# Kernel tuning notes

Hardware: AMD Instinct MI355X
Metric: run time of the kernel (lower is better)

Reference implementation:

```python
import jax, jax.numpy as jnp
import numpy as np

SEQ, D_IN, D_OUT = 8192, 1024, 1024

def setup_inputs() -> dict:
    key = jax.random.key(0)
    kx, kq, kk, kv = jax.random.split(key, 4)
    scale = 1.0 / np.sqrt(D_IN)
    return {
        "x": jax.random.normal(kx, (SEQ, D_IN), dtype=jnp.float32),
        "Wq": jax.random.normal(kq, (D_OUT, D_IN), dtype=jnp.float32) * scale,
        "Wk": jax.random.normal(kk, (D_OUT, D_IN), dtype=jnp.float32) * scale,
        "Wv": jax.random.normal(kv, (D_OUT, D_IN), dtype=jnp.float32) * scale,
    }

def reference(x, Wq, Wk, Wv):
    # nn.Linear: y = x @ W.T (no bias)
    q = x @ Wq.T            # [S, d_out]
    k = x @ Wk.T            # [S, d_out]
    v = x @ Wv.T            # [S, d_out]
    d_k = k.shape[-1]
    scores = (q @ k.T) / jnp.sqrt(jnp.float32(d_k))   # [S, S]
    attn = jax.nn.softmax(scores, axis=-1)
    return attn @ v         # [S, d_out]
```

## Files before the change

### kernel.cpp

```cpp
#include <hip/hip_runtime.h>

typedef unsigned short ushort_t;
typedef __attribute__((ext_vector_type(8))) __bf16 bf16x8;
typedef __attribute__((ext_vector_type(8))) unsigned short ushort8;
typedef __attribute__((ext_vector_type(4))) float f32x4;

#define SEQ 8192
#define DIN 1024
#define DOUT 1024

__device__ __forceinline__ ushort_t f2bf(float f) {
  union { float f; unsigned u; } c; c.f = f;
  unsigned u = c.u;
  return (ushort_t)((u + 0x7fffu + ((u >> 16) & 1u)) >> 16);
}
__device__ __forceinline__ float bf2f(ushort_t h) {
  union { unsigned u; float f; } c; c.u = ((unsigned)h) << 16;
  return c.f;
}

__device__ __forceinline__ void async16(ushort_t* lds, const ushort_t* g) {
  __builtin_amdgcn_global_load_lds(
      (__attribute__((address_space(1))) void*)g,
      (__attribute__((address_space(3))) void*)lds, 16, 0, 0);
}

__global__ __launch_bounds__(256) void cvt_all_kernel(
    const float* __restrict__ x, const float* __restrict__ wq,
    const float* __restrict__ wk, const float* __restrict__ wv,
    ushort_t* __restrict__ xb, ushort_t* __restrict__ wqkb,
    ushort_t* __restrict__ wvb) {
  int b = blockIdx.x;
  const float* src;
  ushort_t* dst;
  int idx;
  if (b < 8192) {
    src = x; dst = xb; idx = b * 256 + threadIdx.x;
  } else {
    int r = b - 8192;
    int w = r >> 10;
    idx = (r & 1023) * 256 + threadIdx.x;
    if (w == 0)      { src = wq; dst = wqkb; }
    else if (w == 1) { src = wk; dst = wqkb + DOUT * DIN; }
    else             { src = wv; dst = wvb; }
  }
  float4 f = ((const float4*)src)[idx];
  ushort4 o;
  o.x = f2bf(f.x); o.y = f2bf(f.y); o.z = f2bf(f.z); o.w = f2bf(f.w);
  ((ushort4*)dst)[idx] = o;
}

template <bool F32OUT, bool SWZ, int BK>
__global__ __launch_bounds__(256) void gemm_bt(const ushort_t* __restrict__ A,
                                               const ushort_t* __restrict__ B,
                                               void* __restrict__ C,
                                               int lda, int ldb, int ldc,
                                               int K, float scale) {
  constexpr int CPR = BK / 8;
  __shared__ ushort_t As[128 * BK];
  __shared__ ushort_t Bs[128 * BK];
  const int t = threadIdx.x;
  const int lane = t & 63;
  const int wave = t >> 6;
  const int wr = wave >> 1, wc = wave & 1;
  const int quad = lane >> 4, r16 = lane & 15;

  int mt, nt;
  if (SWZ) {
    mt = blockIdx.x * (gridDim.y >> 3) + (blockIdx.y >> 3);
    nt = blockIdx.y & 7;
  } else {
    mt = blockIdx.y;
    nt = blockIdx.x;
  }
  const int rowBase = mt * 128;
  const int colBase = nt * 128;

  f32x4 acc[4][4] = {};

  const int nk = K / BK;
  for (int kt = 0; kt < nk; ++kt) {
    #pragma unroll
    for (int i = 0; i < BK / 16; ++i) {
      int c = t + i * 256;
      int row = c / CPR;
      int kq = c & (CPR - 1);
      int kqs = (kq & ~7) | ((kq & 7) ^ (row & 7));
      async16(&As[c * 8], A + (size_t)(rowBase + row) * lda + kt * BK + kqs * 8);
      async16(&Bs[c * 8], B + (size_t)(colBase + row) * ldb + kt * BK + kqs * 8);
    }
    __syncthreads();
    #pragma unroll
    for (int ks = 0; ks < BK / 32; ++ks) {
      bf16x8 af[4], bfr[4];
      #pragma unroll
      for (int mi = 0; mi < 4; ++mi) {
        int row = wr * 64 + mi * 16 + r16;
        int kq = ks * 4 + quad;
        int c = row * CPR + ((kq & ~7) | ((kq & 7) ^ (row & 7)));
        af[mi] = *(const bf16x8*)&As[c * 8];
      }
      #pragma unroll
      for (int ni = 0; ni < 4; ++ni) {
        int row = wc * 64 + ni * 16 + r16;
        int kq = ks * 4 + quad;
        int c = row * CPR + ((kq & ~7) | ((kq & 7) ^ (row & 7)));
        bfr[ni] = *(const bf16x8*)&Bs[c * 8];
      }
      #pragma unroll
      for (int mi = 0; mi < 4; ++mi)
        #pragma unroll
        for (int ni = 0; ni < 4; ++ni)
          acc[mi][ni] = __builtin_amdgcn_mfma_f32_16x16x32_bf16(af[mi], bfr[ni],
                                                                acc[mi][ni], 0, 0, 0);
    }
    __syncthreads();
  }

  #pragma unroll
  for (int mi = 0; mi < 4; ++mi)
    #pragma unroll
    for (int ni = 0; ni < 4; ++ni)
      #pragma unroll
      for (int r = 0; r < 4; ++r) {
        int grow = rowBase + wr * 64 + mi * 16 + quad * 4 + r;
        int gcol = colBase + wc * 64 + ni * 16 + r16;
        float v = acc[mi][ni][r] * scale;
        if (F32OUT)
          ((float*)C)[(size_t)grow * ldc + gcol] = v;
        else
          ((ushort_t*)C)[(size_t)grow * ldc + gcol] = f2bf(v);
      }
}

__global__ __launch_bounds__(256) void softmax_kernel(ushort_t* __restrict__ S) {
  ushort_t* row = S + (size_t)blockIdx.x * SEQ;
  const int t = threadIdx.x;
  __shared__ float red[8];
  float v[32];
  float m = -1e30f;
  #pragma unroll
  for (int j = 0; j < 4; ++j) {
    ushort8 u = ((const ushort8*)row)[t + j * 256];
    #pragma unroll
    for (int e = 0; e < 8; ++e) {
      v[j * 8 + e] = bf2f(u[e]);
      m = fmaxf(m, v[j * 8 + e]);
    }
  }
  #pragma unroll
  for (int off = 32; off >= 1; off >>= 1) m = fmaxf(m, __shfl_xor(m, off, 64));
  if ((t & 63) == 0) red[t >> 6] = m;
  __syncthreads();
  m = fmaxf(fmaxf(red[0], red[1]), fmaxf(red[2], red[3]));
  float s = 0.f;
  #pragma unroll
  for (int i = 0; i < 32; ++i) {
    v[i] = __expf(v[i] - m);
    s += v[i];
  }
  #pragma unroll
  for (int off = 32; off >= 1; off >>= 1) s += __shfl_xor(s, off, 64);
  if ((t & 63) == 0) red[4 + (t >> 6)] = s;
  __syncthreads();
  s = red[4] + red[5] + red[6] + red[7];
  float inv = 1.0f / s;
  #pragma unroll
  for (int j = 0; j < 4; ++j) {
    ushort8 o;
    #pragma unroll
    for (int e = 0; e < 8; ++e) o[e] = f2bf(v[j * 8 + e] * inv);
    ((ushort8*)row)[t + j * 256] = o;
  }
}

extern "C" void kernel_launch(void* const* d_in, const int* in_sizes, int n_in,
                              void* d_out, int out_size, void* d_ws, size_t ws_size,
                              hipStream_t stream) {
  const float* x  = (const float*)d_in[0];
  const float* Wq = (const float*)d_in[1];
  const float* Wk = (const float*)d_in[2];
  const float* Wv = (const float*)d_in[3];
  float* out = (float*)d_out;

  char* p = (char*)d_ws;
  ushort_t* xb   = (ushort_t*)p; p += (size_t)SEQ * DIN * 2;
  ushort_t* wqkb = (ushort_t*)p; p += (size_t)2 * DOUT * DIN * 2;
  ushort_t* wvb  = (ushort_t*)p; p += (size_t)DOUT * DIN * 2;
  ushort_t* qkb  = (ushort_t*)p; p += (size_t)SEQ * 2 * DOUT * 2;
  ushort_t* vtb  = (ushort_t*)p; p += (size_t)DOUT * SEQ * 2;
  ushort_t* Sb   = (ushort_t*)p; p += (size_t)SEQ * SEQ * 2;

  cvt_all_kernel<<<8192 + 3 * 1024, 256, 0, stream>>>(x, Wq, Wk, Wv, xb, wqkb, wvb);

  dim3 blk(256);
  gemm_bt<false, false, 64><<<dim3(2048 / 128, SEQ / 128), blk, 0, stream>>>(
      xb, wqkb, qkb, DIN, DIN, 2 * DOUT, DIN, 1.0f);

  gemm_bt<false, false, 64><<<dim3(SEQ / 128, DOUT / 128), blk, 0, stream>>>(
      wvb, xb, vtb, DIN, DIN, SEQ, DIN, 1.0f);

  gemm_bt<false, false, 64><<<dim3(SEQ / 128, SEQ / 128), blk, 0, stream>>>(
      qkb, qkb + DOUT, Sb, 2 * DOUT, 2 * DOUT, SEQ, DIN, 0.03125f);

  softmax_kernel<<<SEQ, blk, 0, stream>>>(Sb);

  gemm_bt<true, true, 128><<<dim3(DOUT / 128, SEQ / 128), blk, 0, stream>>>(
      Sb, vtb, out, SEQ, SEQ, DOUT, SEQ, 1.0f);
}
```

Before: 489.5 us.

## Fuse softmax into QK^T epilogue and PV normalization, drop softmax kernel

```diff
diff --git a/kernel.cpp b/kernel.cpp
--- a/kernel.cpp
+++ b/kernel.cpp
@@ -9,6 +9,11 @@
 #define DIN 1024
 #define DOUT 1024
 
+#define OM_BF16 0
+#define OM_F32  1
+#define OM_EXP  2
+#define OM_NORM 3
+
 __device__ __forceinline__ ushort_t f2bf(float f) {
   union { float f; unsigned u; } c; c.f = f;
   unsigned u = c.u;
@@ -29,8 +34,13 @@
     const float* __restrict__ x, const float* __restrict__ wq,
     const float* __restrict__ wk, const float* __restrict__ wv,
     ushort_t* __restrict__ xb, ushort_t* __restrict__ wqkb,
-    ushort_t* __restrict__ wvb) {
+    ushort_t* __restrict__ wvb, float* __restrict__ rowsum) {
   int b = blockIdx.x;
+  if (b >= 11264) {
+    int i = (b - 11264) * 256 + threadIdx.x;
+    ((float4*)rowsum)[i] = make_float4(0.f, 0.f, 0.f, 0.f);
+    return;
+  }
   const float* src;
   ushort_t* dst;
   int idx;
@@ -50,12 +60,13 @@
   ((ushort4*)dst)[idx] = o;
 }
 
-template <bool F32OUT, bool SWZ, int BK>
+template <int OUTMODE, int SWZ, int BK>
 __global__ __launch_bounds__(256) void gemm_bt(const ushort_t* __restrict__ A,
                                                const ushort_t* __restrict__ B,
                                                void* __restrict__ C,
                                                int lda, int ldb, int ldc,
-                                               int K, float scale) {
+                                               int K, float scale,
+                                               float* __restrict__ rowsum) {
   constexpr int CPR = BK / 8;
   __shared__ ushort_t As[128 * BK];
   __shared__ ushort_t Bs[128 * BK];
@@ -66,7 +77,7 @@
   const int quad = lane >> 4, r16 = lane & 15;
 
   int mt, nt;
-  if (SWZ) {
+  if (SWZ == 1) {
     mt = blockIdx.x * (gridDim.y >> 3) + (blockIdx.y >> 3);
     nt = blockIdx.y & 7;
   } else {
@@ -117,6 +128,22 @@
     __syncthreads();
   }
 
+  float iv[4][4];
+  float psum[4][4];
+  if (OUTMODE == OM_NORM) {
+    #pragma unroll
+    for (int mi = 0; mi < 4; ++mi)
+      #pragma unroll
+      for (int r = 0; r < 4; ++r)
+        iv[mi][r] = 1.0f / rowsum[rowBase + wr * 64 + mi * 16 + quad * 4 + r];
+  }
+  if (OUTMODE == OM_EXP) {
+    #pragma unroll
+    for (int mi = 0; mi < 4; ++mi)
+      #pragma unroll
+      for (int r = 0; r < 4; ++r) psum[mi][r] = 0.f;
+  }
+
   #pragma unroll
   for (int mi = 0; mi < 4; ++mi)
     #pragma unroll
@@ -125,52 +152,33 @@
       for (int r = 0; r < 4; ++r) {
         int grow = rowBase + wr * 64 + mi * 16 + quad * 4 + r;
         int gcol = colBase + wc * 64 + ni * 16 + r16;
-        float v = acc[mi][ni][r] * scale;
-        if (F32OUT)
-          ((float*)C)[(size_t)grow * ldc + gcol] = v;
-        else
-          ((ushort_t*)C)[(size_t)grow * ldc + gcol] = f2bf(v);
-      }
-}
-
-__global__ __launch_bounds__(256) void softmax_kernel(ushort_t* __restrict__ S) {
-  ushort_t* row = S + (size_t)blockIdx.x * SEQ;
-  const int t = threadIdx.x;
-  __shared__ float red[8];
-  float v[32];
-  float m = -1e30f;
-  #pragma unroll
-  for (int j = 0; j < 4; ++j) {
-    ushort8 u = ((const ushort8*)row)[t + j * 256];
-    #pragma unroll
-    for (int e = 0; e < 8; ++e) {
-      v[j * 8 + e] = bf2f(u[e]);
-      m = fmaxf(m, v[j * 8 + e]);
-    }
-  }
-  #pragma unroll
-  for (int off = 32; off >= 1; off >>= 1) m = fmaxf(m, __shfl_xor(m, off, 64));
-  if ((t & 63) == 0) red[t >> 6] = m;
-  __syncthreads();
-  m = fmaxf(fmaxf(red[0], red[1]), fmaxf(red[2], red[3]));
-  float s = 0.f;
-  #pragma unroll
-  for (int i = 0; i < 32; ++i) {
-    v[i] = __expf(v[i] - m);
-    s += v[i];
-  }
-  #pragma unroll
-  for (int off = 32; off >= 1; off >>= 1) s += __shfl_xor(s, off, 64);
-  if ((t & 63) == 0) red[4 + (t >> 6)] = s;
-  __syncthreads();
-  s = red[4] + red[5] + red[6] + red[7];
-  float inv = 1.0f / s;
-  #pragma unroll
-  for (int j = 0; j < 4; ++j) {
-    ushort8 o;
-    #pragma unroll
-    for (int e = 0; e < 8; ++e) o[e] = f2bf(v[j * 8 + e] * inv);
-    ((ushort8*)row)[t + j * 256] = o;
+        float a = acc[mi][ni][r];
+        if (OUTMODE == OM_F32) {
+          ((float*)C)[(size_t)grow * ldc + gcol] = a * scale;
+        } else if (OUTMODE == OM_BF16) {
+          ((ushort_t*)C)[(size_t)grow * ldc + gcol] = f2bf(a * scale);
+        } else if (OUTMODE == OM_EXP) {
+          float e = __expf(a * scale);
+          psum[mi][r] += e;
+          ((ushort_t*)C)[(size_t)grow * ldc + gcol] = f2bf(e);
+        } else {
+          ((float*)C)[(size_t)grow * ldc + gcol] = a * iv[mi][r];
+        }
+      }
+
+  if (OUTMODE == OM_EXP) {
+    #pragma unroll
+    for (int mi = 0; mi < 4; ++mi)
+      #pragma unroll
+      for (int r = 0; r < 4; ++r) {
+        float s = psum[mi][r];
+        s += __shfl_xor(s, 1, 64);
+        s += __shfl_xor(s, 2, 64);
+        s += __shfl_xor(s, 4, 64);
+        s += __shfl_xor(s, 8, 64);
+        if (r16 == 0)
+          atomicAdd(&rowsum[rowBase + wr * 64 + mi * 16 + quad * 4 + r], s);
+      }
   }
 }
 
@@ -189,22 +197,22 @@
   ushort_t* wvb  = (ushort_t*)p; p += (size_t)DOUT * DIN * 2;
   ushort_t* qkb  = (ushort_t*)p; p += (size_t)SEQ * 2 * DOUT * 2;
   ushort_t* vtb  = (ushort_t*)p; p += (size_t)DOUT * SEQ * 2;
+  float*    rs   = (float*)p;    p += (size_t)SEQ * 4;
   ushort_t* Sb   = (ushort_t*)p; p += (size_t)SEQ * SEQ * 2;
 
-  cvt_all_kernel<<<8192 + 3 * 1024, 256, 0, stream>>>(x, Wq, Wk, Wv, xb, wqkb, wvb);
+  cvt_all_kernel<<<8192 + 3 * 1024 + 8, 256, 0, stream>>>(x, Wq, Wk, Wv, xb, wqkb,
+                                                          wvb, rs);
 
   dim3 blk(256);
-  gemm_bt<false, false, 64><<<dim3(2048 / 128, SEQ / 128), blk, 0, stream>>>(
-      xb, wqkb, qkb, DIN, DIN, 2 * DOUT, DIN, 1.0f);
-
-  gemm_bt<false, false, 64><<<dim3(SEQ / 128, DOUT / 128), blk, 0, stream>>>(
-      wvb, xb, vtb, DIN, DIN, SEQ, DIN, 1.0f);
-
-  gemm_bt<false, false, 64><<<dim3(SEQ / 128, SEQ / 128), blk, 0, stream>>>(
-      qkb, qkb + DOUT, Sb, 2 * DOUT, 2 * DOUT, SEQ, DIN, 0.03125f);
-
-  softmax_kernel<<<SEQ, blk, 0, stream>>>(Sb);
-
-  gemm_bt<true, true, 128><<<dim3(DOUT / 128, SEQ / 128), blk, 0, stream>>>(
-      Sb, vtb, out, SEQ, SEQ, DOUT, SEQ, 1.0f);
-}
+  gemm_bt<OM_BF16, 0, 64><<<dim3(2048 / 128, SEQ / 128), blk, 0, stream>>>(
+      xb, wqkb, qkb, DIN, DIN, 2 * DOUT, DIN, 1.0f, nullptr);
+
+  gemm_bt<OM_BF16, 0, 128><<<dim3(SEQ / 128, DOUT / 128), blk, 0, stream>>>(
+      wvb, xb, vtb, DIN, DIN, SEQ, DIN, 1.0f, nullptr);
+
+  gemm_bt<OM_EXP, 0, 64><<<dim3(SEQ / 128, SEQ / 128), blk, 0, stream>>>(
+      qkb, qkb + DOUT, Sb, 2 * DOUT, 2 * DOUT, SEQ, DIN, 0.03125f, rs);
+
+  gemm_bt<OM_NORM, 1, 128><<<dim3(DOUT / 128, SEQ / 128), blk, 0, stream>>>(
+      Sb, vtb, out, SEQ, SEQ, DOUT, SEQ, 1.0f, rs);
+}
```

Result: faster. 478.5 us (-2.3%).
